# Kernel optimization log

Measured on AMD Instinct MI355X. Metric: run time of the kernel, lower is better.

Reference implementation:

```python
import jax, jax.numpy as jnp
import numpy as np

NC, NW, E, EW = 100000, 500, 600000, 25000
H, L, DFF, CF, WF = 128, 3, 512, 32, 16


def setup_inputs() -> dict:
    key = jax.random.key(0)
    ks = iter(jax.random.split(key, 48))
    def nrm(shape, s=0.05):
        return jax.random.normal(next(ks), shape, jnp.float32) * s
    inp = {}
    inp["cell_x"] = jax.random.normal(next(ks), (NC, CF), jnp.float32)
    inp["well_x"] = jax.random.normal(next(ks), (NW, WF), jnp.float32)
    inp["c2c_edge_index"] = jax.random.randint(next(ks), (2, E), 0, NC)
    inp["c2c_edge_attr"] = jax.random.normal(next(ks), (E, 1), jnp.float32)
    inp["c2w_src"] = jax.random.randint(next(ks), (EW,), 0, NC)
    inp["c2w_dst"] = jax.random.randint(next(ks), (EW,), 0, NW)
    inp["W_cell"] = nrm((CF, H)); inp["b_cell"] = jnp.zeros((H,), jnp.float32)
    inp["W_well"] = nrm((WF, H)); inp["b_well"] = jnp.zeros((H,), jnp.float32)
    inp["W_ee"] = nrm((1, H));   inp["b_ee"] = jnp.zeros((H,), jnp.float32)
    inp["gW"]  = nrm((L, H, H))
    inp["gas"] = nrm((L, H)); inp["gad"] = nrm((L, H)); inp["gae"] = nrm((L, H))
    inp["gWe"] = nrm((L, H, H)); inp["gb"] = jnp.zeros((L, H), jnp.float32)
    inp["n1g"] = jnp.ones((L, H), jnp.float32); inp["n1b"] = jnp.zeros((L, H), jnp.float32)
    inp["fW1"] = nrm((L, H, DFF)); inp["fb1"] = jnp.zeros((L, DFF), jnp.float32)
    inp["fW2"] = nrm((L, DFF, H)); inp["fb2"] = jnp.zeros((L, H), jnp.float32)
    inp["n2g"] = jnp.ones((L, H), jnp.float32); inp["n2b"] = jnp.zeros((L, H), jnp.float32)
    inp["wW"] = nrm((H, H)); inp["was"] = nrm((H,)); inp["wad"] = nrm((H,))
    inp["wb"] = jnp.zeros((H,), jnp.float32)
    inp["mW1"] = nrm((H, H)); inp["mb1"] = jnp.zeros((H,), jnp.float32)
    inp["mW2"] = nrm((H, 75)); inp["mb2"] = jnp.zeros((75,), jnp.float32)
    return inp


def _layer_norm(x, g, b):
    mu = x.mean(-1, keepdims=True)
    v = ((x - mu) ** 2).mean(-1, keepdims=True)
    return (x - mu) * jax.lax.rsqrt(v + 1e-5) * g + b


def _seg_softmax(a, seg, n):
    # numerically stable softmax over edges grouped by destination node
    m = jax.ops.segment_max(a, seg, num_segments=n)
    e = jnp.exp(a - m[seg])
    s = jax.ops.segment_sum(e, seg, num_segments=n)
    s = jnp.where(s == 0, 1.0, s)
    return e / s[seg]


def reference(cell_x, well_x, c2c_edge_index, c2c_edge_attr, c2w_src, c2w_dst,
              W_cell, b_cell, W_well, b_well, W_ee, b_ee,
              gW, gas, gad, gae, gWe, gb,
              n1g, n1b, fW1, fb1, fW2, fb2, n2g, n2b,
              wW, was, wad, wb, mW1, mb1, mW2, mb2):
    src, dst = c2c_edge_index[0], c2c_edge_index[1]
    h = cell_x @ W_cell + b_cell           # [NC, H]
    hw = well_x @ W_well + b_well          # [NW, H]
    ea = c2c_edge_attr @ W_ee + b_ee       # [E, H] embedded edge features
    for i in range(L):
        # GATConv with edge features (heads=1, concat=False, no self loops)
        xn = _layer_norm(h, n1g[i], n1b[i])
        hs = xn @ gW[i]                    # [NC, H]
        alpha = (hs @ gas[i])[src] + (hs @ gad[i])[dst] + (ea @ gWe[i]) @ gae[i]
        alpha = jax.nn.leaky_relu(alpha, 0.2)
        alpha = _seg_softmax(alpha, dst, NC)
        msg = jax.ops.segment_sum(hs[src] * alpha[:, None], dst, num_segments=NC) + gb[i]
        h = h + msg                        # residual (dropout = identity in eval)
        xn = _layer_norm(h, n2g[i], n2b[i])
        h = h + (jax.nn.relu(xn @ fW1[i] + fb1[i]) @ fW2[i] + fb2[i])
    # cell -> well bipartite GATConv (shared lin for src/dst, no edge feats)
    hc = h @ wW                            # [NC, H]
    hwp = hw @ wW                          # [NW, H]
    a = (hc @ was)[c2w_src] + (hwp @ wad)[c2w_dst]
    a = jax.nn.leaky_relu(a, 0.2)
    a = _seg_softmax(a, c2w_dst, NW)
    h_well = jax.ops.segment_sum(hc[c2w_src] * a[:, None], c2w_dst, num_segments=NW) + wb
    out = jax.nn.relu(h_well @ mW1 + mb1) @ mW2 + mb2
    return out.reshape(-1, 3, 25)
```

## Files before the change

kernel.cpp:

```cpp
#include <hip/hip_runtime.h>
#include <hip/hip_bf16.h>

#define NC 100000
#define NW 500
#define NE_CC 600000
#define NE_CW 25000
#define H 128
#define NL 3
#define DFF 512
#define DC 64

typedef __bf16 bf16x8 __attribute__((ext_vector_type(8)));
typedef float f32x4 __attribute__((ext_vector_type(4)));
#define MFMA16(a,b,c) __builtin_amdgcn_mfma_f32_16x16x32_bf16(a,b,c,0,0,0)

__device__ __forceinline__ float wsum(float v){
  #pragma unroll
  for (int o = 32; o; o >>= 1) v += __shfl_xor(v, o, 64);
  return v;
}
__device__ __forceinline__ float gsum16(float v){
  #pragma unroll
  for (int o = 1; o < 16; o <<= 1) v += __shfl_xor(v, o, 64);
  return v;
}
__device__ __forceinline__ float gmax16(float v){
  #pragma unroll
  for (int o = 1; o < 16; o <<= 1) v = fmaxf(v, __shfl_xor(v, o, 64));
  return v;
}

__device__ __forceinline__ void gload16(const void* g, void* l){
  __builtin_amdgcn_global_load_lds(
      (const __attribute__((address_space(1))) void*)g,
      (__attribute__((address_space(3))) void*)l, 16, 0, 0);
}


__global__ void prep_imgGW_k(const float* __restrict__ in, char* __restrict__ img, int nmat){
  int tot = nmat * 16384;
  for (int i = blockIdx.x * 256 + threadIdx.x; i < tot; i += gridDim.x * 256){
    int j = i & 7, lane = (i >> 3) & 63, f = (i >> 9) & 31, l = i >> 14;
    int lr = lane & 15, lk = lane >> 4;
    int ks = f >> 3, nt = f & 7;
    int k = ks * 32 + lk * 8 + j, n = nt * 16 + lr;
    float v = in[(size_t)l * 16384 + (size_t)k * 128 + n];
    *(__hip_bfloat16*)(img + (size_t)l * 32768 + f * 1024 + lane * 16 + j * 2) =
        __float2bfloat16(v);
  }
}
__global__ void prep_imgW1_k(const float* __restrict__ in, char* __restrict__ img){
  int tot = 3 * 65536;
  for (int i = blockIdx.x * 256 + threadIdx.x; i < tot; i += gridDim.x * 256){
    int j = i & 7, lane = (i >> 3) & 63, f = (i >> 9) & 15, ch = (i >> 13) & 7, l = i >> 16;
    int lr = lane & 15, lk = lane >> 4;
    int ks = f >> 2, nt = f & 3;
    int k = ks * 32 + lk * 8 + j, n = ch * 64 + nt * 16 + lr;
    float v = in[(size_t)l * 65536 + (size_t)k * 512 + n];
    *(__hip_bfloat16*)(img + (size_t)(l * 8 + ch) * 16384 + f * 1024 + lane * 16 + j * 2) =
        __float2bfloat16(v);
  }
}
__global__ void prep_imgW2_k(const float* __restrict__ in, char* __restrict__ img){
  int tot = 3 * 65536;
  for (int i = blockIdx.x * 256 + threadIdx.x; i < tot; i += gridDim.x * 256){
    int j = i & 7, lane = (i >> 3) & 63, f = (i >> 9) & 15, ch = (i >> 13) & 7, l = i >> 16;
    int lr = lane & 15, lk = lane >> 4;
    int ks = f >> 3, nt = f & 7;
    int k = ch * 64 + ks * 32 + lk * 8 + j, n = nt * 16 + lr;
    float v = in[(size_t)l * 65536 + (size_t)k * 128 + n];
    *(__hip_bfloat16*)(img + (size_t)(l * 8 + ch) * 16384 + f * 1024 + lane * 16 + j * 2) =
        __float2bfloat16(v);
  }
}

__global__ __launch_bounds__(256) void embed_ln_k(const float* __restrict__ x,
    const float* __restrict__ W, const float* __restrict__ b,
    const float* __restrict__ g, const float* __restrict__ lb,
    float* __restrict__ h, __hip_bfloat16* __restrict__ xn, int M)
{
  int lane = threadIdx.x & 63, wid = threadIdx.x >> 6;
  float w0[32], w1[32];
  #pragma unroll
  for (int k = 0; k < 32; k++){
    w0[k] = W[k * 128 + lane];
    w1[k] = W[k * 128 + 64 + lane];
  }
  float b0 = b[lane], b1 = b[lane + 64];
  float g0 = g[lane], g1 = g[lane + 64];
  float e0 = lb[lane], e1 = lb[lane + 64];
  for (int n = blockIdx.x * 4 + wid; n < M; n += gridDim.x * 4){
    const float4* xr = (const float4*)(x + (size_t)n * 32);
    float xs[32];
    #pragma unroll
    for (int q = 0; q < 8; q++){
      float4 t = xr[q];
      xs[4*q] = t.x; xs[4*q+1] = t.y; xs[4*q+2] = t.z; xs[4*q+3] = t.w;
    }
    float a0 = b0, a1 = b1;
    #pragma unroll
    for (int k = 0; k < 32; k++){ a0 += xs[k] * w0[k]; a1 += xs[k] * w1[k]; }
    h[(size_t)n * H + lane]      = a0;
    h[(size_t)n * H + lane + 64] = a1;
    float mu = wsum(a0 + a1) * (1.f / 128.f);
    float d0 = a0 - mu, d1 = a1 - mu;
    float var = wsum(d0 * d0 + d1 * d1) * (1.f / 128.f);
    float rs = rsqrtf(var + 1e-5f);
    xn[(size_t)n * H + lane]      = __float2bfloat16(d0 * rs * g0 + e0);
    xn[(size_t)n * H + lane + 64] = __float2bfloat16(d1 * rs * g1 + e1);
  }
}

template<int K>
__global__ __launch_bounds__(256) void embed_k(const float* __restrict__ x,
    const float* __restrict__ W, const float* __restrict__ b,
    float* __restrict__ h, int M)
{
  __shared__ float sW[K * 128];
  for (int t = threadIdx.x; t < K * 128; t += 256) sW[t] = W[t];
  __syncthreads();
  int j = threadIdx.x & 127, half = threadIdx.x >> 7;
  float bj = b[j];
  for (int n = blockIdx.x * 2 + half; n < M; n += gridDim.x * 2){
    const float* xr = x + (size_t)n * K;
    float acc = bj;
    #pragma unroll
    for (int k = 0; k < K; k++) acc += xr[k] * sW[k * 128 + j];
    h[(size_t)n * H + j] = acc;
  }
}

__global__ void coeff_k(const float* __restrict__ gWe, const float* __restrict__ gae,
    const float* __restrict__ Wee, const float* __restrict__ bee, float* __restrict__ coeff)
{
  __shared__ float red[4];
  int t = threadIdx.x;
  for (int i = 0; i < NL; i++){
    const float* Wr = gWe + ((size_t)i * H + t) * H;
    const float* ga = gae + (size_t)i * H;
    float w = 0.f;
    for (int k = 0; k < H; k++) w += Wr[k] * ga[k];
    float pc = Wee[t] * w, pd = bee[t] * w;
    pc = wsum(pc); pd = wsum(pd);
    if ((t & 63) == 0){ red[(t >> 6) * 2 + 0] = pc; red[(t >> 6) * 2 + 1] = pd; }
    __syncthreads();
    if (t == 0){ coeff[i] = red[0] + red[2]; coeff[NL + i] = red[1] + red[3]; }
    __syncthreads();
  }
}

__global__ __launch_bounds__(256) void dot2_k(const float* __restrict__ X,
    const float* __restrict__ va, float* __restrict__ oa, int M)
{
  int lane = threadIdx.x & 63, wid = threadIdx.x >> 6;
  int n = blockIdx.x * 4 + wid;
  if (n >= M) return;
  const float* row = X + (size_t)n * H;
  float a = wsum(row[lane] * va[lane] + row[lane + 64] * va[lane + 64]);
  if (lane == 0) oa[n] = a;
}

__global__ __launch_bounds__(512, 4) void gemm_mfma_k(
    const __hip_bfloat16* __restrict__ A, const char* __restrict__ Wimg,
    float* __restrict__ C, __hip_bfloat16* __restrict__ Cbf,
    const float* __restrict__ va, const float* __restrict__ vb,
    float* __restrict__ oa, float* __restrict__ ob, int M)
{
  __shared__ uint4 sW4[2048];
  char* sW = (char*)sW4;
  const int tid = threadIdx.x;
  const int lane = tid & 63, w = tid >> 6;
  const int n0 = blockIdx.x * 128;
  const int rw = w * 16;
  const int lr = lane & 15, lk = lane >> 4;

  {
    int go = w * 1024 + lane * 16;
    #pragma unroll
    for (int q = 0; q < 4; q++)
      gload16(Wimg + q * 8192 + go, sW + q * 8192 + w * 1024);
  }

  const int arow = n0 + rw + lr;
  bf16x8 aX[4];
  if (arow < M){
    #pragma unroll
    for (int ks = 0; ks < 4; ks++)
      aX[ks] = *(const bf16x8*)(A + (size_t)arow * 128 + ks * 32 + lk * 8);
  } else {
    #pragma unroll
    for (int ks = 0; ks < 4; ks++) aX[ks] = (bf16x8){0,0,0,0,0,0,0,0};
  }
  __syncthreads();

  f32x4 acc[8];
  #pragma unroll
  for (int i = 0; i < 8; i++) acc[i] = (f32x4){0.f, 0.f, 0.f, 0.f};
  #pragma unroll
  for (int ks = 0; ks < 4; ks++){
    #pragma unroll
    for (int nt = 0; nt < 8; nt++){
      bf16x8 b = *(const bf16x8*)(sW + ((ks << 3) + nt) * 1024 + (lane << 4));
      acc[nt] = MFMA16(aX[ks], b, acc[nt]);
    }
  }
  #pragma unroll
  for (int nt = 0; nt < 8; nt++){
    int col = nt * 16 + lr;
    #pragma unroll
    for (int r = 0; r < 4; r++){
      int row = n0 + rw + lk * 4 + r;
      if (row < M){
        if (C)   C[(size_t)row * 128 + col] = acc[nt][r];
        if (Cbf) Cbf[(size_t)row * 128 + col] = __float2bfloat16(acc[nt][r]);
      }
    }
  }
  if (va){
    float vac[8], vbc[8];
    #pragma unroll
    for (int nt = 0; nt < 8; nt++){
      vac[nt] = va[nt * 16 + lr];
      vbc[nt] = vb ? vb[nt * 16 + lr] : 0.f;
    }
    #pragma unroll
    for (int r = 0; r < 4; r++){
      float da = 0.f, db = 0.f;
      #pragma unroll
      for (int nt = 0; nt < 8; nt++){
        da += acc[nt][r] * vac[nt];
        db += acc[nt][r] * vbc[nt];
      }
      #pragma unroll
      for (int o = 1; o < 16; o <<= 1){
        da += __shfl_xor(da, o, 64);
        db += __shfl_xor(db, o, 64);
      }
      int row = n0 + rw + lk * 4 + r;
      if (lr == 0 && row < M){
        oa[row] = da;
        if (ob) ob[row] = db;
      }
    }
  }
}

__global__ __launch_bounds__(512, 4) void ffn_mfma_k(
    const __hip_bfloat16* __restrict__ xn, float* __restrict__ h,
    const char* __restrict__ W1img, const float* __restrict__ b1,
    const char* __restrict__ W2img, const float* __restrict__ b2,
    const float* __restrict__ lng, const float* __restrict__ lnb,
    __hip_bfloat16* __restrict__ xout, int mode, int M)
{
  __shared__ uint4 sW1_4[2][1024];
  __shared__ uint4 sW2_4[2][1024];
  __shared__ uint4 sT4[1024];
  char* sT = (char*)sT4;
  const int tid = threadIdx.x;
  const int lane = tid & 63, w = tid >> 6;
  const int n0 = blockIdx.x * 128;
  const int rw = w * 16;
  const int lr = lane & 15, lk = lane >> 4;
  const int go = w * 1024 + lane * 16;
  const int lo = w * 1024;
  char* sTw = sT + w * 2048;

  const int arow = n0 + rw + lr;
  bf16x8 aX[4];
  if (arow < M){
    #pragma unroll
    for (int ks = 0; ks < 4; ks++)
      aX[ks] = *(const bf16x8*)(xn + (size_t)arow * 128 + ks * 32 + lk * 8);
  } else {
    #pragma unroll
    for (int ks = 0; ks < 4; ks++) aX[ks] = (bf16x8){0,0,0,0,0,0,0,0};
  }

  gload16(W1img + go,        (char*)sW1_4[0] + lo);
  gload16(W1img + 8192 + go, (char*)sW1_4[0] + 8192 + lo);
  gload16(W2img + go,        (char*)sW2_4[0] + lo);
  gload16(W2img + 8192 + go, (char*)sW2_4[0] + 8192 + lo);
  asm volatile("s_waitcnt vmcnt(0)" ::: "memory");
  __builtin_amdgcn_s_barrier();

  f32x4 acc2[8];
  #pragma unroll
  for (int i = 0; i < 8; i++) acc2[i] = (f32x4){0.f, 0.f, 0.f, 0.f};

  const int rdA = ((lane ^ ((lane >> 3) & 7)) << 4);

  for (int ch = 0; ch < DFF / DC; ch++){
    const int cur = ch & 1;
    if (ch < DFF / DC - 1){
      const char* g1 = W1img + (size_t)(ch + 1) * 16384;
      const char* g2 = W2img + (size_t)(ch + 1) * 16384;
      char* d1 = (char*)sW1_4[cur ^ 1];
      char* d2 = (char*)sW2_4[cur ^ 1];
      gload16(g1 + go,        d1 + lo);
      gload16(g1 + 8192 + go, d1 + 8192 + lo);
      gload16(g2 + go,        d2 + lo);
      gload16(g2 + 8192 + go, d2 + 8192 + lo);
    }

    const char* W1c = (const char*)sW1_4[cur];
    const char* W2c = (const char*)sW2_4[cur];

    f32x4 acc1[4];
    #pragma unroll
    for (int i = 0; i < 4; i++) acc1[i] = (f32x4){0.f, 0.f, 0.f, 0.f};
    #pragma unroll
    for (int ks = 0; ks < 4; ks++){
      #pragma unroll
      for (int nt = 0; nt < 4; nt++){
        bf16x8 b = *(const bf16x8*)(W1c + ((ks << 2) + nt) * 1024 + (lane << 4));
        acc1[nt] = MFMA16(aX[ks], b, acc1[nt]);
      }
    }
    #pragma unroll
    for (int nt = 0; nt < 4; nt++){
      int col = nt * 16 + lr;
      float bb = b1[ch * DC + col];
      int ksp = col >> 5;
      int qhi = ((col >> 3) & 3) << 4;
      int jb  = (col & 7) << 1;
      #pragma unroll
      for (int r = 0; r < 4; r++){
        int slot = qhi + lk * 4 + r;
        int slotp = slot ^ ((slot >> 3) & 7);
        float v = fmaxf(acc1[nt][r] + bb, 0.f);
        *(__hip_bfloat16*)(sTw + (ksp << 10) + (slotp << 4) + jb) = __float2bfloat16(v);
      }
    }
    asm volatile("s_waitcnt lgkmcnt(0)" ::: "memory");

    #pragma unroll
    for (int ks = 0; ks < 2; ks++){
      bf16x8 a = *(const bf16x8*)(sTw + (ks << 10) + rdA);
      #pragma unroll
      for (int nt = 0; nt < 8; nt++){
        bf16x8 b = *(const bf16x8*)(W2c + ((ks << 3) + nt) * 1024 + (lane << 4));
        acc2[nt] = MFMA16(a, b, acc2[nt]);
      }
    }
    if (ch < DFF / DC - 1){
      asm volatile("s_waitcnt vmcnt(0)" ::: "memory");
      __builtin_amdgcn_s_barrier();
    }
  }

  float b2c[8];
  #pragma unroll
  for (int nt = 0; nt < 8; nt++) b2c[nt] = b2[nt * 16 + lr];

  #pragma unroll
  for (int r = 0; r < 4; r++){
    int row = n0 + rw + lk * 4 + r;
    bool ok = row < M;
    float val[8]; float sum = 0.f;
    #pragma unroll
    for (int nt = 0; nt < 8; nt++){
      int col = nt * 16 + lr;
      float hv = ok ? h[(size_t)row * 128 + col] : 0.f;
      val[nt] = hv + acc2[nt][r] + b2c[nt];
      sum += val[nt];
    }
    if (mode == 0){
      #pragma unroll
      for (int o = 1; o < 16; o <<= 1) sum += __shfl_xor(sum, o, 64);
      float mu = sum * (1.f / 128.f);
      float vs = 0.f;
      #pragma unroll
      for (int nt = 0; nt < 8; nt++){ float d = val[nt] - mu; vs += d * d; }
      #pragma unroll
      for (int o = 1; o < 16; o <<= 1) vs += __shfl_xor(vs, o, 64);
      float rs = rsqrtf(vs * (1.f / 128.f) + 1e-5f);
      #pragma unroll
      for (int nt = 0; nt < 8; nt++){
        int col = nt * 16 + lr;
        if (ok){
          h[(size_t)row * 128 + col] = val[nt];
          xout[(size_t)row * 128 + col] =
              __float2bfloat16((val[nt] - mu) * rs * lng[col] + lnb[col]);
        }
      }
    } else {
      #pragma unroll
      for (int nt = 0; nt < 8; nt++){
        int col = nt * 16 + lr;
        if (ok){
          h[(size_t)row * 128 + col] = val[nt];
          xout[(size_t)row * 128 + col] = __float2bfloat16(val[nt]);
        }
      }
    }
  }
}

__global__ __launch_bounds__(256) void gemm128_k(const float* __restrict__ A,
    const float* __restrict__ Bm, float* __restrict__ C, int M)
{
  __shared__ float sB[32 * 128];
  __shared__ float sA[64 * 33];
  const int tid = threadIdx.x;
  const int n0 = blockIdx.x * 64;
  const int j4 = (tid & 31) * 4;
  const int rB = (tid >> 5) * 8;
  float acc[8][4];
  #pragma unroll
  for (int r = 0; r < 8; r++){ acc[r][0]=acc[r][1]=acc[r][2]=acc[r][3]=0.f; }
  for (int kc = 0; kc < 128; kc += 32){
    for (int t = tid; t < 4096; t += 256){
      int kk = t >> 7, j = t & 127;
      sB[kk * 128 + j] = Bm[(size_t)(kc + kk) * H + j];
    }
    for (int t = tid; t < 2048; t += 256){
      int n = t >> 5, kk = t & 31; int row = n0 + n;
      sA[n * 33 + kk] = (row < M) ? A[(size_t)row * H + kc + kk] : 0.f;
    }
    __syncthreads();
    #pragma unroll 8
    for (int kk = 0; kk < 32; kk++){
      float4 bv = *(const float4*)&sB[kk * 128 + j4];
      #pragma unroll
      for (int r = 0; r < 8; r++){
        float av = sA[(rB + r) * 33 + kk];
        acc[r][0] += av * bv.x; acc[r][1] += av * bv.y;
        acc[r][2] += av * bv.z; acc[r][3] += av * bv.w;
      }
    }
    __syncthreads();
  }
  #pragma unroll
  for (int r = 0; r < 8; r++){
    int row = n0 + rB + r;
    if (row < M){
      float4 o; o.x = acc[r][0]; o.y = acc[r][1]; o.z = acc[r][2]; o.w = acc[r][3];
      *(float4*)&C[(size_t)row * H + j4] = o;
    }
  }
}

__global__ void count_k(const int* __restrict__ dst, int* __restrict__ cnt, int NE){
  int e = blockIdx.x * 256 + threadIdx.x;
  if (e < NE) atomicAdd(&cnt[dst[e]], 1);
}
__global__ void scan1_k(const int* __restrict__ in, int* __restrict__ out,
                        int* __restrict__ bsum, int N){
  __shared__ int sd[256];
  int tid = threadIdx.x;
  int base = blockIdx.x * 1024 + tid * 4;
  int v0 = (base + 0 < N) ? in[base + 0] : 0;
  int v1 = (base + 1 < N) ? in[base + 1] : 0;
  int v2 = (base + 2 < N) ? in[base + 2] : 0;
  int v3 = (base + 3 < N) ? in[base + 3] : 0;
  sd[tid] = v0 + v1 + v2 + v3;
  __syncthreads();
  for (int off = 1; off < 256; off <<= 1){
    int t = (tid >= off) ? sd[tid - off] : 0;
    __syncthreads();
    sd[tid] += t;
    __syncthreads();
  }
  int run = (tid > 0) ? sd[tid - 1] : 0;
  run += v0; if (base + 0 < N) out[base + 0] = run;
  run += v1; if (base + 1 < N) out[base + 1] = run;
  run += v2; if (base + 2 < N) out[base + 2] = run;
  run += v3; if (base + 3 < N) out[base + 3] = run;
  if (tid == 255) bsum[blockIdx.x] = sd[255];
}
__global__ void scan2_k(int* __restrict__ bs, int NB){
  __shared__ int sd[256];
  int tid = threadIdx.x;
  int base = tid * 4;
  int v0 = (base + 0 < NB) ? bs[base + 0] : 0;
  int v1 = (base + 1 < NB) ? bs[base + 1] : 0;
  int v2 = (base + 2 < NB) ? bs[base + 2] : 0;
  int v3 = (base + 3 < NB) ? bs[base + 3] : 0;
  sd[tid] = v0 + v1 + v2 + v3;
  __syncthreads();
  for (int off = 1; off < 256; off <<= 1){
    int t = (tid >= off) ? sd[tid - off] : 0;
    __syncthreads();
    sd[tid] += t;
    __syncthreads();
  }
  int run = (tid > 0) ? sd[tid - 1] : 0;
  run += v0; if (base + 0 < NB) bs[base + 0] = run;
  run += v1; if (base + 1 < NB) bs[base + 1] = run;
  run += v2; if (base + 2 < NB) bs[base + 2] = run;
  run += v3; if (base + 3 < NB) bs[base + 3] = run;
}
__global__ void scan3_k(int* __restrict__ out, const int* __restrict__ bsum, int N){
  int b = blockIdx.x;
  if (b == 0) return;
  int add = bsum[b - 1];
  int i = b * 1024 + threadIdx.x * 4;
  #pragma unroll
  for (int j = 0; j < 4; j++) if (i + j < N) out[i + j] += add;
}
__global__ void initfill_k(const int* __restrict__ incl, int* __restrict__ fill, int N){
  int i = blockIdx.x * 256 + threadIdx.x;
  if (i < N) fill[i] = (i == 0) ? 0 : incl[i - 1];
}
__global__ void fill_k(const int* __restrict__ dst, int* __restrict__ fill,
                       int* __restrict__ csr, int NE){
  int e = blockIdx.x * 256 + threadIdx.x;
  if (e < NE){
    int p = atomicAdd(&fill[dst[e]], 1);
    csr[p] = e;
  }
}

__global__ __launch_bounds__(256) void gat_k(
    const int* __restrict__ incl, const int* __restrict__ csr,
    const int* __restrict__ src, const float* __restrict__ attr,
    const float* __restrict__ coeff, int ci,
    const float* __restrict__ as_, const float* __restrict__ ad_,
    const __hip_bfloat16* __restrict__ X, float* __restrict__ hout,
    const float* __restrict__ gb, const float* __restrict__ g,
    const float* __restrict__ b, __hip_bfloat16* __restrict__ xn,
    int M, int residual)
{
  int lane = threadIdx.x & 63, wid = threadIdx.x >> 6;
  int grp = lane >> 4, gl = lane & 15;
  int n = blockIdx.x * 16 + wid * 4 + grp;
  if (n >= M) return;
  int beg = (n == 0) ? 0 : incl[n - 1];
  int end = incl[n];
  float c0 = 0.f, c1 = 0.f;
  if (attr){ c0 = coeff[ci]; c1 = coeff[NL + ci]; }
  float adn = ad_[n];
  const int gbase = grp << 4;
  float m = -1e30f, s = 0.f;
  float acc[8];
  #pragma unroll
  for (int i = 0; i < 8; i++) acc[i] = 0.f;

  for (int base = beg; base < end; base += 16){
    int idx = base + gl;
    bool valid = idx < end;
    int e = valid ? csr[idx] : 0;
    int sv = valid ? src[e] : 0;
    float a = -1e30f;
    if (valid){
      a = as_[sv] + adn;
      if (attr) a += attr[e] * c0 + c1;
      a = (a > 0.f) ? a : 0.2f * a;
    }
    float cm = gmax16(a);
    float nm = fmaxf(m, cm);
    float sc = expf(m - nm);
    #pragma unroll
    for (int i = 0; i < 8; i++) acc[i] *= sc;
    s *= sc;
    float p = valid ? expf(a - nm) : 0.f;
    s += gsum16(p);
    m = nm;
    int cnt = min(16, end - base);
    for (int t = 0; t < cnt; t++){
      float pt = __shfl(p, gbase + t, 64);
      int st = __shfl(sv, gbase + t, 64);
      uint4 u = *(const uint4*)(X + (size_t)st * H + gl * 8);
      acc[0] += pt * __uint_as_float(u.x << 16);
      acc[1] += pt * __uint_as_float(u.x & 0xffff0000u);
      acc[2] += pt * __uint_as_float(u.y << 16);
      acc[3] += pt * __uint_as_float(u.y & 0xffff0000u);
      acc[4] += pt * __uint_as_float(u.z << 16);
      acc[5] += pt * __uint_as_float(u.z & 0xffff0000u);
      acc[6] += pt * __uint_as_float(u.w << 16);
      acc[7] += pt * __uint_as_float(u.w & 0xffff0000u);
    }
  }
  float inv = (s == 0.f) ? 0.f : 1.f / s;
  int j0 = gl * 8;
  if (residual){
    float4 h0 = *(float4*)&hout[(size_t)n * H + j0];
    float4 h1 = *(float4*)&hout[(size_t)n * H + j0 + 4];
    float4 g0 = *(const float4*)&gb[j0];
    float4 g1 = *(const float4*)&gb[j0 + 4];
    float hv[8];
    hv[0] = h0.x + acc[0] * inv + g0.x; hv[1] = h0.y + acc[1] * inv + g0.y;
    hv[2] = h0.z + acc[2] * inv + g0.z; hv[3] = h0.w + acc[3] * inv + g0.w;
    hv[4] = h1.x + acc[4] * inv + g1.x; hv[5] = h1.y + acc[5] * inv + g1.y;
    hv[6] = h1.z + acc[6] * inv + g1.z; hv[7] = h1.w + acc[7] * inv + g1.w;
    float localsum = 0.f;
    #pragma unroll
    for (int i = 0; i < 8; i++) localsum += hv[i];
    float mu = gsum16(localsum) * (1.f / H);
    float vs = 0.f;
    #pragma unroll
    for (int i = 0; i < 8; i++){ float d = hv[i] - mu; vs += d * d; }
    float var = gsum16(vs) * (1.f / H);
    float rs = rsqrtf(var + 1e-5f);
    float4 o0, o1;
    o0.x = hv[0]; o0.y = hv[1]; o0.z = hv[2]; o0.w = hv[3];
    o1.x = hv[4]; o1.y = hv[5]; o1.z = hv[6]; o1.w = hv[7];
    *(float4*)&hout[(size_t)n * H + j0] = o0;
    *(float4*)&hout[(size_t)n * H + j0 + 4] = o1;
    float4 gg0 = *(const float4*)&g[j0];
    float4 gg1 = *(const float4*)&g[j0 + 4];
    float4 bb0 = *(const float4*)&b[j0];
    float4 bb1 = *(const float4*)&b[j0 + 4];
    float xo[8];
    xo[0] = (hv[0]-mu)*rs*gg0.x + bb0.x; xo[1] = (hv[1]-mu)*rs*gg0.y + bb0.y;
    xo[2] = (hv[2]-mu)*rs*gg0.z + bb0.z; xo[3] = (hv[3]-mu)*rs*gg0.w + bb0.w;
    xo[4] = (hv[4]-mu)*rs*gg1.x + bb1.x; xo[5] = (hv[5]-mu)*rs*gg1.y + bb1.y;
    xo[6] = (hv[6]-mu)*rs*gg1.z + bb1.z; xo[7] = (hv[7]-mu)*rs*gg1.w + bb1.w;
    uint4 ow;
    unsigned* owp = (unsigned*)&ow;
    #pragma unroll
    for (int i = 0; i < 4; i++){
      __hip_bfloat16 lo = __float2bfloat16(xo[2*i]);
      __hip_bfloat16 hi = __float2bfloat16(xo[2*i+1]);
      owp[i] = ((unsigned)(*(unsigned short*)&hi) << 16) | (*(unsigned short*)&lo);
    }
    *(uint4*)((char*)xn + ((size_t)n * H + j0) * 2) = ow;
  } else {
    float4 o0, o1;
    o0.x = acc[0]*inv; o0.y = acc[1]*inv; o0.z = acc[2]*inv; o0.w = acc[3]*inv;
    o1.x = acc[4]*inv; o1.y = acc[5]*inv; o1.z = acc[6]*inv; o1.w = acc[7]*inv;
    *(float4*)&hout[(size_t)n * H + j0] = o0;
    *(float4*)&hout[(size_t)n * H + j0 + 4] = o1;
  }
}

__global__ __launch_bounds__(128) void mlp_k(const float* __restrict__ hwell,
    const float* __restrict__ wb, const float* __restrict__ mW1,
    const float* __restrict__ mb1, const float* __restrict__ mW2,
    const float* __restrict__ mb2, float* __restrict__ out)
{
  __shared__ float sH[128], sT[128];
  int n = blockIdx.x, j = threadIdx.x;
  sH[j] = hwell[(size_t)n * H + j] + wb[j];
  __syncthreads();
  float a = mb1[j];
  for (int k = 0; k < 128; k++) a += sH[k] * mW1[k * 128 + j];
  sT[j] = fmaxf(a, 0.f);
  __syncthreads();
  if (j < 75){
    float o = mb2[j];
    for (int k = 0; k < 128; k++) o += sT[k] * mW2[k * 75 + j];
    out[(size_t)n * 75 + j] = o;
  }
}

extern "C" void kernel_launch(void* const* d_in, const int* in_sizes, int n_in,
                              void* d_out, int out_size, void* d_ws, size_t ws_size,
                              hipStream_t stream)
{
  (void)in_sizes; (void)n_in; (void)out_size; (void)ws_size;
  const float* cell_x = (const float*)d_in[0];
  const float* well_x = (const float*)d_in[1];
  const int*   eidx   = (const int*)d_in[2];
  const float* eattr  = (const float*)d_in[3];
  const int*   wsrc   = (const int*)d_in[4];
  const int*   wdst   = (const int*)d_in[5];
  const float* W_cell = (const float*)d_in[6];
  const float* b_cell = (const float*)d_in[7];
  const float* W_well = (const float*)d_in[8];
  const float* b_well = (const float*)d_in[9];
  const float* W_ee   = (const float*)d_in[10];
  const float* b_ee   = (const float*)d_in[11];
  const float* gW     = (const float*)d_in[12];
  const float* gas    = (const float*)d_in[13];
  const float* gad    = (const float*)d_in[14];
  const float* gae    = (const float*)d_in[15];
  const float* gWe    = (const float*)d_in[16];
  const float* gb     = (const float*)d_in[17];
  const float* n1g    = (const float*)d_in[18];
  const float* n1b    = (const float*)d_in[19];
  const float* fW1    = (const float*)d_in[20];
  const float* fb1    = (const float*)d_in[21];
  const float* fW2    = (const float*)d_in[22];
  const float* fb2    = (const float*)d_in[23];
  const float* n2g    = (const float*)d_in[24];
  const float* n2b    = (const float*)d_in[25];
  const float* wW     = (const float*)d_in[26];
  const float* was    = (const float*)d_in[27];
  const float* wad    = (const float*)d_in[28];
  const float* wb     = (const float*)d_in[29];
  const float* mW1    = (const float*)d_in[30];
  const float* mb1    = (const float*)d_in[31];
  const float* mW2    = (const float*)d_in[32];
  const float* mb2    = (const float*)d_in[33];

  const int* src = eidx;
  const int* dst = eidx + NE_CC;

  char* wsb = (char*)d_ws;
  size_t off = 0;
  auto alloc = [&](size_t bytes) -> void* {
    void* p = wsb + off; off += (bytes + 255) & ~(size_t)255; return p;
  };
  float* h      = (float*)alloc((size_t)NC * H * 4);
  __hip_bfloat16* xnbf = (__hip_bfloat16*)alloc((size_t)NC * H * 2);
  __hip_bfloat16* hsbf = (__hip_bfloat16*)alloc((size_t)NC * H * 2);
  float* as_    = (float*)alloc((size_t)NC * 4);
  float* ad_    = (float*)alloc((size_t)NC * 4);
  float* hw     = (float*)alloc((size_t)NW * H * 4);
  float* hwp    = (float*)alloc((size_t)NW * H * 4);
  float* hwell  = (float*)alloc((size_t)NW * H * 4);
  float* coeff  = (float*)alloc(64);
  char* gWimg = (char*)alloc((size_t)NL * 32768);
  char* wWimg = (char*)alloc(32768);
  char* W1img = (char*)alloc((size_t)NL * 131072);
  char* W2img = (char*)alloc((size_t)NL * 131072);
  int* cntC  = (int*)alloc((size_t)NC * 4);
  int* inclC = (int*)alloc((size_t)NC * 4);
  int* fillC = (int*)alloc((size_t)NC * 4);
  int* csrC  = (int*)alloc((size_t)NE_CC * 4);
  int* inclW = (int*)alloc((size_t)NW * 4);
  int* fillW = (int*)alloc((size_t)NW * 4);
  int* csrW  = (int*)alloc((size_t)NE_CW * 4);
  int* bsum  = (int*)alloc(1024 * 4);

  const int eBlocks  = (NE_CC + 255) / 256;
  const int ewBlocks = (NE_CW + 255) / 256;
  const int NBC = (NC + 1023) / 1024;
  const int NBW = (NW + 1023) / 1024;

  hipMemsetAsync(cntC, 0, (size_t)NC * 4, stream);
  count_k<<<eBlocks, 256, 0, stream>>>(dst, cntC, NE_CC);
  scan1_k<<<NBC, 256, 0, stream>>>(cntC, inclC, bsum, NC);
  scan2_k<<<1, 256, 0, stream>>>(bsum, NBC);
  scan3_k<<<NBC, 256, 0, stream>>>(inclC, bsum, NC);
  initfill_k<<<(NC + 255) / 256, 256, 0, stream>>>(inclC, fillC, NC);
  fill_k<<<eBlocks, 256, 0, stream>>>(dst, fillC, csrC, NE_CC);
  hipMemsetAsync(fillW, 0, (size_t)NW * 4, stream);
  count_k<<<ewBlocks, 256, 0, stream>>>(wdst, fillW, NE_CW);
  scan1_k<<<NBW, 256, 0, stream>>>(fillW, inclW, bsum, NW);
  scan2_k<<<1, 256, 0, stream>>>(bsum, NBW);
  scan3_k<<<NBW, 256, 0, stream>>>(inclW, bsum, NW);
  initfill_k<<<(NW + 255) / 256, 256, 0, stream>>>(inclW, fillW, NW);
  fill_k<<<ewBlocks, 256, 0, stream>>>(wdst, fillW, csrW, NE_CW);

  prep_imgGW_k<<<96, 256, 0, stream>>>(gW, gWimg, NL);
  prep_imgGW_k<<<32, 256, 0, stream>>>(wW, wWimg, 1);
  prep_imgW1_k<<<768, 256, 0, stream>>>(fW1, W1img);
  prep_imgW2_k<<<768, 256, 0, stream>>>(fW2, W2img);

  embed_ln_k<<<1024, 256, 0, stream>>>(cell_x, W_cell, b_cell, n1g, n1b, h, xnbf, NC);
  embed_k<16><<<250, 256, 0, stream>>>(well_x, W_well, b_well, hw, NW);
  coeff_k<<<1, 128, 0, stream>>>(gWe, gae, W_ee, b_ee, coeff);

  const int mfmaBlocks = (NC + 127) / 128;
  const int gatBlocks = (NC + 15) / 16;

  for (int i = 0; i < NL; i++){
    gemm_mfma_k<<<mfmaBlocks, 512, 0, stream>>>(xnbf, gWimg + (size_t)i * 32768,
        nullptr, hsbf, gas + i * H, gad + i * H, as_, ad_, NC);
    gat_k<<<gatBlocks, 256, 0, stream>>>(inclC, csrC, src, eattr, coeff, i,
        as_, ad_, hsbf, h, gb + i * H, n2g + i * H, n2b + i * H, xnbf, NC, 1);
    int last = (i == NL - 1);
    ffn_mfma_k<<<mfmaBlocks, 512, 0, stream>>>(xnbf, h,
        W1img + (size_t)i * 131072, fb1 + (size_t)i * DFF,
        W2img + (size_t)i * 131072, fb2 + (size_t)i * H,
        n1g + ((i + 1) % NL) * H, n1b + ((i + 1) % NL) * H,
        xnbf, last ? 1 : 0, NC);
  }

  gemm_mfma_k<<<mfmaBlocks, 512, 0, stream>>>(xnbf, wWimg,
      nullptr, hsbf, was, nullptr, as_, nullptr, NC);
  gemm128_k<<<(NW + 63) / 64, 256, 0, stream>>>(hw, wW, hwp, NW);
  dot2_k<<<(NW + 3) / 4, 256, 0, stream>>>(hwp, wad, ad_, NW);
  gat_k<<<(NW + 15) / 16, 256, 0, stream>>>(inclW, csrW, wsrc, nullptr, coeff, 0,
      as_, ad_, hsbf, hwell, nullptr, nullptr, nullptr, nullptr, NW, 0);
  mlp_k<<<NW, 128, 0, stream>>>(hwell, wb, mW1, mb1, mW2, mb2, (float*)d_out);
}
```

Before: 645.5 us.

## Fuse next-layer GAT projection GEMM into FFN kernel epilogue

The FFN kernel now applies the following LayerNorm, stages the normalized rows in shared memory, and runs the next layer's GAT projection (or the final cell-to-well projection) with MFMA inside the same kernel. It also writes the attention dot products directly. This removes the separate gemm_mfma launches and the global round trip of the normalized activations. In exchange the FFN epilogue gets heavier, uses more registers and reuses the shared-memory buffers, which could reduce occupancy.

```diff
diff --git a/kernel.cpp b/kernel.cpp
--- a/kernel.cpp
+++ b/kernel.cpp
@@ -250,7 +250,10 @@
     const char* __restrict__ W1img, const float* __restrict__ b1,
     const char* __restrict__ W2img, const float* __restrict__ b2,
     const float* __restrict__ lng, const float* __restrict__ lnb,
-    __hip_bfloat16* __restrict__ xout, int mode, int M)
+    const char* __restrict__ Wg,
+    const float* __restrict__ va, const float* __restrict__ vb,
+    float* __restrict__ oa, float* __restrict__ ob,
+    __hip_bfloat16* __restrict__ Cbf, int mode, int M)
 {
   __shared__ uint4 sW1_4[2][1024];
   __shared__ uint4 sW2_4[2][1024];
@@ -300,6 +303,11 @@
       gload16(g1 + 8192 + go, d1 + 8192 + lo);
       gload16(g2 + go,        d2 + lo);
       gload16(g2 + 8192 + go, d2 + 8192 + lo);
+    } else {
+      gload16(Wg + go,         (char*)sW1_4[0] + lo);
+      gload16(Wg + 8192 + go,  (char*)sW1_4[0] + 8192 + lo);
+      gload16(Wg + 16384 + go, (char*)sW2_4[0] + lo);
+      gload16(Wg + 24576 + go, (char*)sW2_4[0] + 8192 + lo);
     }
 
     const char* W1c = (const char*)sW1_4[cur];
@@ -348,9 +356,23 @@
     }
   }
 
+  asm volatile("s_waitcnt vmcnt(0)" ::: "memory");
+  __builtin_amdgcn_s_barrier();
+
+  char* aimg = (w < 4) ? ((char*)sW1_4[1] + w * 4096)
+                       : ((char*)sW2_4[1] + (w - 4) * 4096);
+
   float b2c[8];
   #pragma unroll
   for (int nt = 0; nt < 8; nt++) b2c[nt] = b2[nt * 16 + lr];
+  float lngc[8], lnbc[8];
+  if (mode == 0){
+    #pragma unroll
+    for (int nt = 0; nt < 8; nt++){
+      lngc[nt] = lng[nt * 16 + lr];
+      lnbc[nt] = lnb[nt * 16 + lr];
+    }
+  }
 
   #pragma unroll
   for (int r = 0; r < 4; r++){
@@ -364,33 +386,80 @@
       val[nt] = hv + acc2[nt][r] + b2c[nt];
       sum += val[nt];
     }
+    float mu = 0.f, rs = 1.f;
     if (mode == 0){
       #pragma unroll
       for (int o = 1; o < 16; o <<= 1) sum += __shfl_xor(sum, o, 64);
-      float mu = sum * (1.f / 128.f);
+      mu = sum * (1.f / 128.f);
       float vs = 0.f;
       #pragma unroll
       for (int nt = 0; nt < 8; nt++){ float d = val[nt] - mu; vs += d * d; }
       #pragma unroll
       for (int o = 1; o < 16; o <<= 1) vs += __shfl_xor(vs, o, 64);
-      float rs = rsqrtf(vs * (1.f / 128.f) + 1e-5f);
+      rs = rsqrtf(vs * (1.f / 128.f) + 1e-5f);
+    }
+    #pragma unroll
+    for (int nt = 0; nt < 8; nt++){
+      int col = nt * 16 + lr;
+      if (mode == 0 && ok) h[(size_t)row * 128 + col] = val[nt];
+      float xo = (mode == 0) ? ((val[nt] - mu) * rs * lngc[nt] + lnbc[nt]) : val[nt];
+      int lanep = ((((nt & 1) << 1) + (lr >> 3)) << 4) + (lk << 2) + r;
+      *(__hip_bfloat16*)(aimg + ((nt >> 1) << 10) + (lanep << 4) + ((lr & 7) << 1)) =
+          __float2bfloat16(xo);
+    }
+  }
+  asm volatile("s_waitcnt lgkmcnt(0)" ::: "memory");
+
+  bf16x8 aG[4];
+  #pragma unroll
+  for (int ks = 0; ks < 4; ks++)
+    aG[ks] = *(const bf16x8*)(aimg + (ks << 10) + (lane << 4));
+  f32x4 accG[8];
+  #pragma unroll
+  for (int i = 0; i < 8; i++) accG[i] = (f32x4){0.f, 0.f, 0.f, 0.f};
+  #pragma unroll
+  for (int ks = 0; ks < 4; ks++){
+    #pragma unroll
+    for (int nt = 0; nt < 8; nt++){
+      const char* bptr = (ks < 2)
+          ? ((const char*)sW1_4[0] + (((ks << 3) + nt) << 10) + (lane << 4))
+          : ((const char*)sW2_4[0] + ((((ks - 2) << 3) + nt) << 10) + (lane << 4));
+      accG[nt] = MFMA16(aG[ks], *(const bf16x8*)bptr, accG[nt]);
+    }
+  }
+  #pragma unroll
+  for (int nt = 0; nt < 8; nt++){
+    int col = nt * 16 + lr;
+    #pragma unroll
+    for (int r = 0; r < 4; r++){
+      int row = n0 + rw + lk * 4 + r;
+      if (row < M) Cbf[(size_t)row * 128 + col] = __float2bfloat16(accG[nt][r]);
+    }
+  }
+  {
+    float vac[8], vbc[8];
+    #pragma unroll
+    for (int nt = 0; nt < 8; nt++){
+      vac[nt] = va[nt * 16 + lr];
+      vbc[nt] = vb ? vb[nt * 16 + lr] : 0.f;
+    }
+    #pragma unroll
+    for (int r = 0; r < 4; r++){
+      float da = 0.f, db = 0.f;
       #pragma unroll
       for (int nt = 0; nt < 8; nt++){
-        int col = nt * 16 + lr;
-        if (ok){
-          h[(size_t)row * 128 + col] = val[nt];
-          xout[(size_t)row * 128 + col] =
-              __float2bfloat16((val[nt] - mu) * rs * lng[col] + lnb[col]);
-        }
-      }
-    } else {
-      #pragma unroll
-      for (int nt = 0; nt < 8; nt++){
-        int col = nt * 16 + lr;
-        if (ok){
-          h[(size_t)row * 128 + col] = val[nt];
-          xout[(size_t)row * 128 + col] = __float2bfloat16(val[nt]);
-        }
+        da += accG[nt][r] * vac[nt];
+        db += accG[nt][r] * vbc[nt];
+      }
+      #pragma unroll
+      for (int o = 1; o < 16; o <<= 1){
+        da += __shfl_xor(da, o, 64);
+        db += __shfl_xor(db, o, 64);
+      }
+      int row = n0 + rw + lk * 4 + r;
+      if (lr == 0 && row < M){
+        oa[row] = da;
+        if (ob) ob[row] = db;
       }
     }
   }
@@ -746,21 +815,28 @@
   const int mfmaBlocks = (NC + 127) / 128;
   const int gatBlocks = (NC + 15) / 16;
 
+  gemm_mfma_k<<<mfmaBlocks, 512, 0, stream>>>(xnbf, gWimg,
+      nullptr, hsbf, gas, gad, as_, ad_, NC);
+
   for (int i = 0; i < NL; i++){
-    gemm_mfma_k<<<mfmaBlocks, 512, 0, stream>>>(xnbf, gWimg + (size_t)i * 32768,
-        nullptr, hsbf, gas + i * H, gad + i * H, as_, ad_, NC);
     gat_k<<<gatBlocks, 256, 0, stream>>>(inclC, csrC, src, eattr, coeff, i,
         as_, ad_, hsbf, h, gb + i * H, n2g + i * H, n2b + i * H, xnbf, NC, 1);
-    int last = (i == NL - 1);
-    ffn_mfma_k<<<mfmaBlocks, 512, 0, stream>>>(xnbf, h,
-        W1img + (size_t)i * 131072, fb1 + (size_t)i * DFF,
-        W2img + (size_t)i * 131072, fb2 + (size_t)i * H,
-        n1g + ((i + 1) % NL) * H, n1b + ((i + 1) % NL) * H,
-        xnbf, last ? 1 : 0, NC);
-  }
-
-  gemm_mfma_k<<<mfmaBlocks, 512, 0, stream>>>(xnbf, wWimg,
-      nullptr, hsbf, was, nullptr, as_, nullptr, NC);
+    if (i < NL - 1){
+      ffn_mfma_k<<<mfmaBlocks, 512, 0, stream>>>(xnbf, h,
+          W1img + (size_t)i * 131072, fb1 + (size_t)i * DFF,
+          W2img + (size_t)i * 131072, fb2 + (size_t)i * H,
+          n1g + (i + 1) * H, n1b + (i + 1) * H,
+          gWimg + (size_t)(i + 1) * 32768,
+          gas + (i + 1) * H, gad + (i + 1) * H, as_, ad_, hsbf, 0, NC);
+    } else {
+      ffn_mfma_k<<<mfmaBlocks, 512, 0, stream>>>(xnbf, h,
+          W1img + (size_t)i * 131072, fb1 + (size_t)i * DFF,
+          W2img + (size_t)i * 131072, fb2 + (size_t)i * H,
+          n1g, n1b,
+          wWimg, was, nullptr, as_, nullptr, hsbf, 1, NC);
+    }
+  }
+
   gemm128_k<<<(NW + 63) / 64, 256, 0, stream>>>(hw, wW, hwp, NW);
   dot2_k<<<(NW + 3) / 4, 256, 0, stream>>>(hwp, wad, ad_, NW);
   gat_k<<<(NW + 15) / 16, 256, 0, stream>>>(inclW, csrW, wsrc, nullptr, coeff, 0,
```

Result: faster. 610.9 us (-5.4%).
